# Performance work log

Measured on AMD Instinct MI355X. Metric: run time of the kernel, lower is better.

Reference implementation:

```python
import jax, jax.numpy as jnp
import numpy as np
from jax import ops as jops

N_NODES = 100000
N_EDGES = 1600000
NEG_SLOPE = 0.2
LN_EPS = 1e-5


def setup_inputs() -> dict:
    key = jax.random.key(0)
    ks = jax.random.split(key, 12)
    inp = {
        "x": jax.random.normal(ks[0], (N_NODES, 4), jnp.float32),
        "edge_index": jax.random.randint(ks[1], (2, N_EDGES), 0, N_NODES, jnp.int64 if jax.config.jax_enable_x64 else jnp.int32),
        # layer 1: GATv2Conv(4, 16, heads=4)
        "W1l": jax.random.normal(ks[2], (4, 64), jnp.float32) * 0.5,
        "W1r": jax.random.normal(ks[3], (4, 64), jnp.float32) * 0.5,
        "a1": jax.random.normal(ks[4], (4, 16), jnp.float32) * 0.5,  # [heads, out]
        "b1": jax.random.normal(ks[5], (64,), jnp.float32) * 0.1,
        "g1": jnp.ones((64,), jnp.float32),
        "be1": jnp.zeros((64,), jnp.float32),
        # layer 2: GATv2Conv(64, 32, heads=1)
        "W2l": jax.random.normal(ks[6], (64, 32), jnp.float32) * 0.125,
        "W2r": jax.random.normal(ks[7], (64, 32), jnp.float32) * 0.125,
        "a2": jax.random.normal(ks[8], (1, 32), jnp.float32) * 0.5,
        "b2": jax.random.normal(ks[9], (32,), jnp.float32) * 0.1,
        "g2": jnp.ones((32,), jnp.float32),
        "be2": jnp.zeros((32,), jnp.float32),
    }
    return inp


def _add_self_loops(edge_index, n):
    loop = jnp.arange(n, dtype=edge_index.dtype)
    return jnp.concatenate([edge_index, jnp.stack([loop, loop])], axis=1)


def _gatv2(x, src, dst, Wl, Wr, att, bias, heads, out_ch, n):
    # x: [N, F]; Wl/Wr: [F, heads*out_ch]; att: [heads, out_ch]
    xl = (x @ Wl).reshape(n, heads, out_ch)  # source transform
    xr = (x @ Wr).reshape(n, heads, out_ch)  # target transform
    e = xl[src] + xr[dst]                     # [E, H, C]
    e = jnp.where(e >= 0, e, NEG_SLOPE * e)   # LeakyReLU(0.2)
    logits = jnp.einsum('ehc,hc->eh', e, att)  # [E, H]
    # segment softmax over destination node
    m = jops.segment_max(logits, dst, num_segments=n)  # [N, H]
    ex = jnp.exp(logits - m[dst])
    denom = jops.segment_sum(ex, dst, num_segments=n)  # [N, H]
    alpha = ex / denom[dst]                            # [E, H]
    out = jops.segment_sum(alpha[:, :, None] * xl[src], dst, num_segments=n)  # [N, H, C]
    return out.reshape(n, heads * out_ch) + bias


def _layernorm(x, g, b):
    mu = jnp.mean(x, axis=-1, keepdims=True)
    var = jnp.mean(jnp.square(x - mu), axis=-1, keepdims=True)
    return (x - mu) * jax.lax.rsqrt(var + LN_EPS) * g + b


def reference(x, edge_index, W1l, W1r, a1, b1, g1, be1, W2l, W2r, a2, b2, g2, be2):
    n = x.shape[0]
    ei = _add_self_loops(edge_index, n)
    src, dst = ei[0], ei[1]
    h = _gatv2(x, src, dst, W1l, W1r, a1, b1, heads=4, out_ch=16, n=n)
    h = _layernorm(h, g1, be1)
    h = jnp.where(h > 0, h, jnp.expm1(h))  # ELU
    h = _gatv2(h, src, dst, W2l, W2r, a2, b2, heads=1, out_ch=32, n=n)
    h = _layernorm(h, g2, be2)
    return h
```

## Files before the change

### kernel.cpp

```cpp
#include <hip/hip_runtime.h>
#include <math.h>

#define NN 100000
#define E0 1600000
#define ETOT (E0 + NN)
#define NEG 0.2f

#define NB 512
#define BS 196
#define CHUNK 4096
#define PPT 16
#define MAXP 4096

__device__ __forceinline__ float leaky(float v) { return fmaxf(v, NEG * v); }

__global__ void k_bhist(const int* __restrict__ ei, int* __restrict__ bcnt) {
    __shared__ int h[NB];
    int tid = threadIdx.x;
    for (int i = tid; i < NB; i += 256) h[i] = 0;
    __syncthreads();
    int stride = gridDim.x * 256;
    for (int e = blockIdx.x * 256 + tid; e < E0; e += stride)
        atomicAdd(&h[ei[E0 + e] / BS], 1);
    __syncthreads();
    for (int i = tid; i < NB; i += 256)
        if (h[i]) atomicAdd(&bcnt[i], h[i]);
}

__global__ void k_bscan(const int* __restrict__ bcnt, int* __restrict__ boff,
                        int* __restrict__ srcsBase, int* __restrict__ cursor) {
    __shared__ int s[NB];
    int tid = threadIdx.x;
    int v = bcnt[tid];
    s[tid] = v;
    __syncthreads();
    for (int off = 1; off < NB; off <<= 1) {
        int t = (tid >= off) ? s[tid - off] : 0;
        __syncthreads();
        s[tid] += t;
        __syncthreads();
    }
    int excl = s[tid] - v;
    boff[tid] = excl;
    cursor[tid] = excl;
    int n0 = tid * BS;
    if (n0 > NN) n0 = NN;
    srcsBase[tid] = excl + n0;
}

__global__ void k_bin(const int* __restrict__ ei, int* __restrict__ cursor,
                      int2* __restrict__ binned) {
    __shared__ int hist[NB];
    __shared__ int basesh[NB];
    int tid = threadIdx.x;
    long long cbase = (long long)blockIdx.x * CHUNK;
    for (int i = tid; i < NB; i += 256) hist[i] = 0;
    __syncthreads();
    int srcv[PPT], dstv[PPT], rank[PPT], bkt[PPT];
#pragma unroll
    for (int k = 0; k < PPT; ++k) {
        long long e = cbase + k * 256 + tid;
        if (e < E0) {
            int s_ = ei[e];
            int d_ = ei[E0 + e];
            int b = d_ / BS;
            rank[k] = atomicAdd(&hist[b], 1);
            srcv[k] = s_;
            dstv[k] = d_;
            bkt[k] = b;
        } else {
            bkt[k] = -1;
        }
    }
    __syncthreads();
    for (int i = tid; i < NB; i += 256)
        if (hist[i] > 0) basesh[i] = atomicAdd(&cursor[i], hist[i]);
    __syncthreads();
#pragma unroll
    for (int k = 0; k < PPT; ++k)
        if (bkt[k] >= 0) {
            int2 p;
            p.x = srcv[k];
            p.y = dstv[k];
            binned[basesh[bkt[k]] + rank[k]] = p;
        }
}

__global__ void k_bfin(const int2* __restrict__ binned, const int* __restrict__ bcnt,
                       const int* __restrict__ boff, const int* __restrict__ srcsBase,
                       int* __restrict__ rs, int* __restrict__ srcs) {
    int b = blockIdx.x;
    int n0 = b * BS;
    if (n0 >= NN) return;
    int nd = NN - n0;
    if (nd > BS) nd = BS;
    int cnt = bcnt[b];
    if (cnt > MAXP) cnt = MAXP;
    int base = boff[b];
    int sb = srcsBase[b];
    __shared__ int ldsCnt[256];
    __shared__ int scanA[256];
    __shared__ int rowOffE[256];
    __shared__ int stage[MAXP + BS];
    int tid = threadIdx.x;
    ldsCnt[tid] = 0;
    __syncthreads();
    int srcv[PPT], dl_[PPT], rk_[PPT];
#pragma unroll
    for (int k = 0; k < PPT; ++k) {
        int i = k * 256 + tid;
        if (i < cnt) {
            int2 p = binned[base + i];
            int dl = p.y - n0;
            rk_[k] = atomicAdd(&ldsCnt[dl], 1);
            srcv[k] = p.x;
            dl_[k] = dl;
        } else {
            dl_[k] = -1;
        }
    }
    __syncthreads();
    int v = (tid < nd) ? ldsCnt[tid] + 1 : 0;
    scanA[tid] = v;
    __syncthreads();
    for (int off = 1; off < 256; off <<= 1) {
        int t = (tid >= off) ? scanA[tid - off] : 0;
        __syncthreads();
        scanA[tid] += t;
        __syncthreads();
    }
    rowOffE[tid] = scanA[tid] - v;
    __syncthreads();
    if (tid < nd) {
        int e = rowOffE[tid];
        rs[n0 + tid] = sb + e;
        stage[e] = n0 + tid;
    }
    __syncthreads();
#pragma unroll
    for (int k = 0; k < PPT; ++k)
        if (dl_[k] >= 0) stage[rowOffE[dl_[k]] + 1 + rk_[k]] = srcv[k];
    __syncthreads();
    int tot = cnt + nd;
    for (int i = tid; i < tot; i += 256) srcs[sb + i] = stage[i];
}

__global__ void k_linr(const float* __restrict__ x, const float* __restrict__ Wr,
                       float* __restrict__ xr1) {
    int t = blockIdx.x * blockDim.x + threadIdx.x;
    if (t >= NN * 16) return;
    int n = t >> 4;
    int j = (t & 15) << 2;
    const float4 xv = *(const float4*)(x + (long long)n * 4);
    float4 a = {0.f, 0.f, 0.f, 0.f};
#pragma unroll
    for (int k = 0; k < 4; ++k) {
        float4 w = *(const float4*)(Wr + k * 64 + j);
        float xk = k == 0 ? xv.x : k == 1 ? xv.y : k == 2 ? xv.z : xv.w;
        a.x += xk * w.x; a.y += xk * w.y;
        a.z += xk * w.z; a.w += xk * w.w;
    }
    *(float4*)(xr1 + (long long)n * 64 + j) = a;
}

__global__ void k_gat1(
        const float* __restrict__ x, const float* __restrict__ Wl,
        const float* __restrict__ xr1, const float* __restrict__ att,
        const int* __restrict__ rs, const int* __restrict__ srcs,
        const float* __restrict__ b, const float* __restrict__ g,
        const float* __restrict__ be, float* __restrict__ h) {
    int lane = threadIdx.x & 63;
    int wave = (blockIdx.x * blockDim.x + threadIdx.x) >> 6;
    int nwaves = (gridDim.x * blockDim.x) >> 6;
    int e_i = lane >> 3;
    int sub = lane & 7;
    float wl[4][8], at[8];
#pragma unroll
    for (int k = 0; k < 4; ++k)
#pragma unroll
        for (int j = 0; j < 8; ++j) wl[k][j] = Wl[k * 64 + sub * 8 + j];
#pragma unroll
    for (int j = 0; j < 8; ++j) at[j] = att[sub * 8 + j];

    for (int n = wave; n < NN; n += nwaves) {
        const float4 r0 = *(const float4*)(xr1 + (long long)n * 64 + sub * 8);
        const float4 r1 = *(const float4*)(xr1 + (long long)n * 64 + sub * 8 + 4);
        float xrd[8] = {r0.x, r0.y, r0.z, r0.w, r1.x, r1.y, r1.z, r1.w};
        int beg = rs[n];
        int end = (n == NN - 1) ? ETOT : rs[n + 1];
        float acc4[4] = {0.f, 0.f, 0.f, 0.f};
        float den = 0.f;
        int slot = beg + e_i;
        bool valid = slot < end;
        int s = srcs[valid ? slot : beg];
        float4 xa = *(const float4*)(x + (long long)s * 4);
        for (int base = beg; base < end; base += 8) {
            int nslot = base + 8 + e_i;
            bool nvalid = nslot < end;
            int ns = srcs[nvalid ? nslot : beg];
            float4 xn = *(const float4*)(x + (long long)ns * 4);
            float p = 0.f;
#pragma unroll
            for (int j = 0; j < 8; ++j) {
                float t = xa.x * wl[0][j] + xa.y * wl[1][j] + xa.z * wl[2][j] +
                          xa.w * wl[3][j];
                float u = t + xrd[j];
                u = fmaxf(u, NEG * u);
                p += u * at[j];
            }
            p += __shfl_xor(p, 1);
            float ex = valid ? __expf(p) : 0.f;
            den += ex;
            acc4[0] += ex * xa.x;
            acc4[1] += ex * xa.y;
            acc4[2] += ex * xa.z;
            acc4[3] += ex * xa.w;
            xa = xn;
            valid = nvalid;
        }
#pragma unroll
        for (int m = 8; m <= 32; m <<= 1) {
#pragma unroll
            for (int k = 0; k < 4; ++k) acc4[k] += __shfl_xor(acc4[k], m);
            den += __shfl_xor(den, m);
        }
        int cf = sub * 8 + e_i;
        float v = (acc4[0] * Wl[cf] + acc4[1] * Wl[64 + cf] +
                   acc4[2] * Wl[128 + cf] + acc4[3] * Wl[192 + cf]) / den + b[cf];
        float s1 = v;
#pragma unroll
        for (int m = 1; m < 64; m <<= 1) s1 += __shfl_xor(s1, m);
        float mu = s1 * (1.f / 64.f);
        float c = v - mu;
        float sq = c * c;
#pragma unroll
        for (int m = 1; m < 64; m <<= 1) sq += __shfl_xor(sq, m);
        float y = c * rsqrtf(sq * (1.f / 64.f) + 1e-5f) * g[cf] + be[cf];
        h[(long long)n * 64 + cf] = y > 0.f ? y : expm1f(y);
    }
}

__global__ void k_lin2(const float* __restrict__ h, const float* __restrict__ Wl,
                       const float* __restrict__ Wr, float* __restrict__ xl2,
                       float* __restrict__ xr2) {
    __shared__ float wl_s[2048];
    __shared__ float wr_s[2048];
    for (int i = threadIdx.x; i < 2048; i += blockDim.x) {
        wl_s[i] = Wl[i];
        wr_s[i] = Wr[i];
    }
    __syncthreads();
    int t = blockIdx.x * blockDim.x + threadIdx.x;
    if (t >= NN * 32) return;
    int n = t >> 5, j = t & 31;
    const float* hr = h + (long long)n * 64;
    float al = 0.f, ar = 0.f;
#pragma unroll 8
    for (int k = 0; k < 64; ++k) {
        float hv = hr[k];
        al += hv * wl_s[k * 32 + j];
        ar += hv * wr_s[k * 32 + j];
    }
    xl2[(long long)n * 32 + j] = al;
    xr2[(long long)n * 32 + j] = ar;
}

__global__ void k_gat2(
        const float* __restrict__ xl2, const float* __restrict__ xr2,
        const float* __restrict__ att, const int* __restrict__ rs,
        const int* __restrict__ srcs, const float* __restrict__ b,
        const float* __restrict__ g, const float* __restrict__ be,
        float* __restrict__ out) {
    int lane = threadIdx.x & 63;
    int wave = (blockIdx.x * blockDim.x + threadIdx.x) >> 6;
    int nwaves = (gridDim.x * blockDim.x) >> 6;
    int e_i = lane >> 3;
    int cg = lane & 7;
    float at[4];
#pragma unroll
    for (int j = 0; j < 4; ++j) at[j] = att[cg * 4 + j];

    for (int n = wave; n < NN; n += nwaves) {
        const float4 xr4 = *(const float4*)(xr2 + (long long)n * 32 + cg * 4);
        float xrd[4] = {xr4.x, xr4.y, xr4.z, xr4.w};
        int beg = rs[n];
        int end = (n == NN - 1) ? ETOT : rs[n + 1];
        float acc[4] = {0.f, 0.f, 0.f, 0.f};
        float den = 0.f;
        int slot = beg + e_i;
        bool valid = slot < end;
        int s = srcs[valid ? slot : beg];
        float4 xa = *(const float4*)(xl2 + (long long)s * 32 + cg * 4);
        for (int base = beg; base < end; base += 8) {
            int nslot = base + 8 + e_i;
            bool nvalid = nslot < end;
            int ns = srcs[nvalid ? nslot : beg];
            float4 xn = *(const float4*)(xl2 + (long long)ns * 32 + cg * 4);
            float p = 0.f;
#pragma unroll
            for (int j = 0; j < 4; ++j) {
                float xls = j == 0 ? xa.x : j == 1 ? xa.y : j == 2 ? xa.z : xa.w;
                float u = xls + xrd[j];
                u = fmaxf(u, NEG * u);
                p += u * at[j];
            }
            p += __shfl_xor(p, 1);
            p += __shfl_xor(p, 2);
            p += __shfl_xor(p, 4);
            float ex = valid ? __expf(p) : 0.f;
            den += ex;
            acc[0] += ex * xa.x;
            acc[1] += ex * xa.y;
            acc[2] += ex * xa.z;
            acc[3] += ex * xa.w;
            xa = xn;
            valid = nvalid;
        }
#pragma unroll
        for (int m = 8; m <= 32; m <<= 1) {
#pragma unroll
            for (int j = 0; j < 4; ++j) acc[j] += __shfl_xor(acc[j], m);
            den += __shfl_xor(den, m);
        }
        int e3 = e_i & 3;
        float v = acc[0];
#pragma unroll
        for (int j = 1; j < 4; ++j) v = (e3 == j) ? acc[j] : v;
        int cf = cg * 4 + e3;
        v = v / den + b[cf];
        float s1 = v;
#pragma unroll
        for (int m = 1; m < 64; m <<= 1) s1 += __shfl_xor(s1, m);
        float mu = s1 * (1.f / 64.f);
        float cc = v - mu;
        float sq = cc * cc;
#pragma unroll
        for (int m = 1; m < 64; m <<= 1) sq += __shfl_xor(sq, m);
        float y = cc * rsqrtf(sq * (1.f / 64.f) + 1e-5f) * g[cf] + be[cf];
        if (e_i < 4) out[(long long)n * 32 + cf] = y;
    }
}

extern "C" void kernel_launch(void* const* d_in, const int* in_sizes, int n_in,
                              void* d_out, int out_size, void* d_ws, size_t ws_size,
                              hipStream_t stream) {
    const float* x   = (const float*)d_in[0];
    const int*   ei  = (const int*)d_in[1];
    const float* W1l = (const float*)d_in[2];
    const float* W1r = (const float*)d_in[3];
    const float* a1  = (const float*)d_in[4];
    const float* b1  = (const float*)d_in[5];
    const float* g1  = (const float*)d_in[6];
    const float* be1 = (const float*)d_in[7];
    const float* W2l = (const float*)d_in[8];
    const float* W2r = (const float*)d_in[9];
    const float* a2  = (const float*)d_in[10];
    const float* b2  = (const float*)d_in[11];
    const float* g2  = (const float*)d_in[12];
    const float* be2 = (const float*)d_in[13];
    float* out = (float*)d_out;

    float* ws = (float*)d_ws;
    float* h   = ws;
    float* xr1 = ws + 6400000;
    float* xl2 = ws + 6400000;
    float* xr2 = ws + 9600000;
    int2* binned = (int2*)ws;
    int* ib        = (int*)(ws + 12800000);
    int* rs        = ib;
    int* srcs      = ib + 100000;
    int* bcnt      = ib + 1800000;
    int* boff      = ib + 1800000 + NB;
    int* srcsBase  = ib + 1800000 + 2 * NB;
    int* cursor    = ib + 1800000 + 3 * NB;

    hipMemsetAsync(bcnt, 0, NB * sizeof(int), stream);
    k_bhist<<<256, 256, 0, stream>>>(ei, bcnt);
    k_bscan<<<1, NB, 0, stream>>>(bcnt, boff, srcsBase, cursor);
    k_bin<<<(E0 + CHUNK - 1) / CHUNK, 256, 0, stream>>>(ei, cursor, binned);
    k_bfin<<<NB, 256, 0, stream>>>(binned, bcnt, boff, srcsBase, rs, srcs);
    k_linr<<<(NN * 16 + 255) / 256, 256, 0, stream>>>(x, W1r, xr1);

    k_gat1<<<2048, 256, 0, stream>>>(x, W1l, xr1, a1, rs, srcs, b1, g1, be1, h);
    k_lin2<<<(NN * 32 + 255) / 256, 256, 0, stream>>>(h, W2l, W2r, xl2, xr2);
    k_gat2<<<2048, 256, 0, stream>>>(xl2, xr2, a2, rs, srcs, b2, g2, be2, out);
}
```

Before: 239.1 us.

## Use packed FP32 math and prescaled source offsets in GAT edge loops

Rewrites the per-edge inner loops of both GAT kernels to use v_pk_fma/v_pk_mul/v_pk_add on float pairs, roughly halving the VALU instruction count for the projection, LeakyReLU and accumulation. Source indices are stored prescaled by 16 so gather addresses need no multiply. A sentinel rs[NN] is added to remove the last-node branch, and srcs is padded with zeroed entries so the prefetch can read past the end without clamping. This trades inline asm and workspace offset changes for fewer ALU and address ops in the gather-bound loops.

```diff
diff --git a/kernel.cpp b/kernel.cpp
--- a/kernel.cpp
+++ b/kernel.cpp
@@ -12,7 +12,29 @@
 #define PPT 16
 #define MAXP 4096
 
-__device__ __forceinline__ float leaky(float v) { return fmaxf(v, NEG * v); }
+typedef __attribute__((ext_vector_type(2))) float f32x2;
+
+__device__ __forceinline__ f32x2 pk_fma(f32x2 a, f32x2 b, f32x2 c) {
+    f32x2 d;
+    asm("v_pk_fma_f32 %0, %1, %2, %3" : "=v"(d) : "v"(a), "v"(b), "v"(c));
+    return d;
+}
+__device__ __forceinline__ f32x2 pk_mul(f32x2 a, f32x2 b) {
+    f32x2 d;
+    asm("v_pk_mul_f32 %0, %1, %2" : "=v"(d) : "v"(a), "v"(b));
+    return d;
+}
+__device__ __forceinline__ f32x2 pk_add(f32x2 a, f32x2 b) {
+    f32x2 d;
+    asm("v_pk_add_f32 %0, %1, %2" : "=v"(d) : "v"(a), "v"(b));
+    return d;
+}
+__device__ __forceinline__ f32x2 pk_max(f32x2 a, f32x2 b) {
+    f32x2 d;
+    d[0] = fmaxf(a[0], b[0]);
+    d[1] = fmaxf(a[1], b[1]);
+    return d;
+}
 
 __global__ void k_bhist(const int* __restrict__ ei, int* __restrict__ bcnt) {
     __shared__ int h[NB];
@@ -28,7 +50,8 @@
 }
 
 __global__ void k_bscan(const int* __restrict__ bcnt, int* __restrict__ boff,
-                        int* __restrict__ srcsBase, int* __restrict__ cursor) {
+                        int* __restrict__ srcsBase, int* __restrict__ cursor,
+                        int* __restrict__ rs) {
     __shared__ int s[NB];
     int tid = threadIdx.x;
     int v = bcnt[tid];
@@ -46,6 +69,7 @@
     int n0 = tid * BS;
     if (n0 > NN) n0 = NN;
     srcsBase[tid] = excl + n0;
+    if (tid == 0) rs[NN] = ETOT;
 }
 
 __global__ void k_bin(const int* __restrict__ ei, int* __restrict__ cursor,
@@ -142,7 +166,7 @@
         if (dl_[k] >= 0) stage[rowOffE[dl_[k]] + 1 + rk_[k]] = srcv[k];
     __syncthreads();
     int tot = cnt + nd;
-    for (int i = tid; i < tot; i += 256) srcs[sb + i] = stage[i];
+    for (int i = tid; i < tot; i += 256) srcs[sb + i] = stage[i] << 4;
 }
 
 __global__ void k_linr(const float* __restrict__ x, const float* __restrict__ Wr,
@@ -166,7 +190,7 @@
 __global__ void k_gat1(
         const float* __restrict__ x, const float* __restrict__ Wl,
         const float* __restrict__ xr1, const float* __restrict__ att,
-        const int* __restrict__ rs, const int* __restrict__ srcs,
+        const int* __restrict__ rs, const int* __restrict__ srcs16,
         const float* __restrict__ b, const float* __restrict__ g,
         const float* __restrict__ be, float* __restrict__ h) {
     int lane = threadIdx.x & 63;
@@ -174,50 +198,61 @@
     int nwaves = (gridDim.x * blockDim.x) >> 6;
     int e_i = lane >> 3;
     int sub = lane & 7;
-    float wl[4][8], at[8];
+    f32x2 wl2[4][4], at2[4];
 #pragma unroll
     for (int k = 0; k < 4; ++k)
 #pragma unroll
-        for (int j = 0; j < 8; ++j) wl[k][j] = Wl[k * 64 + sub * 8 + j];
-#pragma unroll
-    for (int j = 0; j < 8; ++j) at[j] = att[sub * 8 + j];
+        for (int jp = 0; jp < 4; ++jp)
+            wl2[k][jp] = *(const f32x2*)(Wl + k * 64 + sub * 8 + jp * 2);
+#pragma unroll
+    for (int jp = 0; jp < 4; ++jp)
+        at2[jp] = *(const f32x2*)(att + sub * 8 + jp * 2);
+    const f32x2 neg2 = {NEG, NEG};
+    const char* xb = (const char*)x;
 
     for (int n = wave; n < NN; n += nwaves) {
-        const float4 r0 = *(const float4*)(xr1 + (long long)n * 64 + sub * 8);
-        const float4 r1 = *(const float4*)(xr1 + (long long)n * 64 + sub * 8 + 4);
-        float xrd[8] = {r0.x, r0.y, r0.z, r0.w, r1.x, r1.y, r1.z, r1.w};
+        f32x2 xrd2[4];
+#pragma unroll
+        for (int jp = 0; jp < 4; ++jp)
+            xrd2[jp] = *(const f32x2*)(xr1 + (long long)n * 64 + sub * 8 + jp * 2);
         int beg = rs[n];
-        int end = (n == NN - 1) ? ETOT : rs[n + 1];
-        float acc4[4] = {0.f, 0.f, 0.f, 0.f};
+        int end = rs[n + 1];
+        int rem = end - beg;
+        const int* sp = srcs16 + beg + e_i;
+        int left = rem - e_i;
+        f32x2 acc01 = {0.f, 0.f}, acc23 = {0.f, 0.f};
         float den = 0.f;
-        int slot = beg + e_i;
-        bool valid = slot < end;
-        int s = srcs[valid ? slot : beg];
-        float4 xa = *(const float4*)(x + (long long)s * 4);
-        for (int base = beg; base < end; base += 8) {
-            int nslot = base + 8 + e_i;
-            bool nvalid = nslot < end;
-            int ns = srcs[nvalid ? nslot : beg];
-            float4 xn = *(const float4*)(x + (long long)ns * 4);
-            float p = 0.f;
-#pragma unroll
-            for (int j = 0; j < 8; ++j) {
-                float t = xa.x * wl[0][j] + xa.y * wl[1][j] + xa.z * wl[2][j] +
-                          xa.w * wl[3][j];
-                float u = t + xrd[j];
-                u = fmaxf(u, NEG * u);
-                p += u * at[j];
+        int s16 = sp[0];
+        float4 xa = *(const float4*)(xb + (unsigned)s16);
+        int nit = (rem + 7) >> 3;
+        for (int it = 0; it < nit; ++it) {
+            int s16n = sp[8];
+            sp += 8;
+            float4 xn = *(const float4*)(xb + (unsigned)s16n);
+            f32x2 xx = {xa.x, xa.x}, xy = {xa.y, xa.y};
+            f32x2 xz = {xa.z, xa.z}, xw = {xa.w, xa.w};
+            f32x2 p2 = {0.f, 0.f};
+#pragma unroll
+            for (int jp = 0; jp < 4; ++jp) {
+                f32x2 t = pk_fma(xx, wl2[0][jp], xrd2[jp]);
+                t = pk_fma(xy, wl2[1][jp], t);
+                t = pk_fma(xz, wl2[2][jp], t);
+                t = pk_fma(xw, wl2[3][jp], t);
+                f32x2 u = pk_max(t, pk_mul(t, neg2));
+                p2 = pk_fma(u, at2[jp], p2);
             }
+            float p = p2[0] + p2[1];
             p += __shfl_xor(p, 1);
-            float ex = valid ? __expf(p) : 0.f;
+            float ex = (left > 0) ? __expf(p) : 0.f;
+            left -= 8;
             den += ex;
-            acc4[0] += ex * xa.x;
-            acc4[1] += ex * xa.y;
-            acc4[2] += ex * xa.z;
-            acc4[3] += ex * xa.w;
+            f32x2 ee = {ex, ex};
+            f32x2 a01 = {xa.x, xa.y}, a23 = {xa.z, xa.w};
+            acc01 = pk_fma(ee, a01, acc01);
+            acc23 = pk_fma(ee, a23, acc23);
             xa = xn;
-            valid = nvalid;
-        }
+        }
+        float acc4[4] = {acc01[0], acc01[1], acc23[0], acc23[1]};
 #pragma unroll
         for (int m = 8; m <= 32; m <<= 1) {
 #pragma unroll
@@ -268,7 +303,7 @@
 __global__ void k_gat2(
         const float* __restrict__ xl2, const float* __restrict__ xr2,
         const float* __restrict__ att, const int* __restrict__ rs,
-        const int* __restrict__ srcs, const float* __restrict__ b,
+        const int* __restrict__ srcs16, const float* __restrict__ b,
         const float* __restrict__ g, const float* __restrict__ be,
         float* __restrict__ out) {
     int lane = threadIdx.x & 63;
@@ -276,46 +311,49 @@
     int nwaves = (gridDim.x * blockDim.x) >> 6;
     int e_i = lane >> 3;
     int cg = lane & 7;
-    float at[4];
-#pragma unroll
-    for (int j = 0; j < 4; ++j) at[j] = att[cg * 4 + j];
+    f32x2 at2[2];
+    at2[0] = *(const f32x2*)(att + cg * 4);
+    at2[1] = *(const f32x2*)(att + cg * 4 + 2);
+    const f32x2 neg2 = {NEG, NEG};
+    const char* xlb = (const char*)xl2 + cg * 16;
 
     for (int n = wave; n < NN; n += nwaves) {
-        const float4 xr4 = *(const float4*)(xr2 + (long long)n * 32 + cg * 4);
-        float xrd[4] = {xr4.x, xr4.y, xr4.z, xr4.w};
+        f32x2 xrd0 = *(const f32x2*)(xr2 + (long long)n * 32 + cg * 4);
+        f32x2 xrd1 = *(const f32x2*)(xr2 + (long long)n * 32 + cg * 4 + 2);
         int beg = rs[n];
-        int end = (n == NN - 1) ? ETOT : rs[n + 1];
-        float acc[4] = {0.f, 0.f, 0.f, 0.f};
+        int end = rs[n + 1];
+        int rem = end - beg;
+        const int* sp = srcs16 + beg + e_i;
+        int left = rem - e_i;
+        f32x2 acc01 = {0.f, 0.f}, acc23 = {0.f, 0.f};
         float den = 0.f;
-        int slot = beg + e_i;
-        bool valid = slot < end;
-        int s = srcs[valid ? slot : beg];
-        float4 xa = *(const float4*)(xl2 + (long long)s * 32 + cg * 4);
-        for (int base = beg; base < end; base += 8) {
-            int nslot = base + 8 + e_i;
-            bool nvalid = nslot < end;
-            int ns = srcs[nvalid ? nslot : beg];
-            float4 xn = *(const float4*)(xl2 + (long long)ns * 32 + cg * 4);
-            float p = 0.f;
-#pragma unroll
-            for (int j = 0; j < 4; ++j) {
-                float xls = j == 0 ? xa.x : j == 1 ? xa.y : j == 2 ? xa.z : xa.w;
-                float u = xls + xrd[j];
-                u = fmaxf(u, NEG * u);
-                p += u * at[j];
-            }
+        int s16 = sp[0];
+        float4 xa = *(const float4*)(xlb + (unsigned)(s16 << 3));
+        int nit = (rem + 7) >> 3;
+        for (int it = 0; it < nit; ++it) {
+            int s16n = sp[8];
+            sp += 8;
+            float4 xn = *(const float4*)(xlb + (unsigned)(s16n << 3));
+            f32x2 a01 = {xa.x, xa.y}, a23 = {xa.z, xa.w};
+            f32x2 t0 = pk_add(a01, xrd0);
+            f32x2 t1 = pk_add(a23, xrd1);
+            f32x2 u0 = pk_max(t0, pk_mul(t0, neg2));
+            f32x2 u1 = pk_max(t1, pk_mul(t1, neg2));
+            f32x2 p2 = pk_mul(u0, at2[0]);
+            p2 = pk_fma(u1, at2[1], p2);
+            float p = p2[0] + p2[1];
             p += __shfl_xor(p, 1);
             p += __shfl_xor(p, 2);
             p += __shfl_xor(p, 4);
-            float ex = valid ? __expf(p) : 0.f;
+            float ex = (left > 0) ? __expf(p) : 0.f;
+            left -= 8;
             den += ex;
-            acc[0] += ex * xa.x;
-            acc[1] += ex * xa.y;
-            acc[2] += ex * xa.z;
-            acc[3] += ex * xa.w;
+            f32x2 ee = {ex, ex};
+            acc01 = pk_fma(ee, a01, acc01);
+            acc23 = pk_fma(ee, a23, acc23);
             xa = xn;
-            valid = nvalid;
-        }
+        }
+        float acc[4] = {acc01[0], acc01[1], acc23[0], acc23[1]};
 #pragma unroll
         for (int m = 8; m <= 32; m <<= 1) {
 #pragma unroll
@@ -368,15 +406,16 @@
     int2* binned = (int2*)ws;
     int* ib        = (int*)(ws + 12800000);
     int* rs        = ib;
-    int* srcs      = ib + 100000;
-    int* bcnt      = ib + 1800000;
-    int* boff      = ib + 1800000 + NB;
-    int* srcsBase  = ib + 1800000 + 2 * NB;
-    int* cursor    = ib + 1800000 + 3 * NB;
+    int* srcs      = ib + 100001;
+    int* bcnt      = ib + 1800100;
+    int* boff      = ib + 1800100 + NB;
+    int* srcsBase  = ib + 1800100 + 2 * NB;
+    int* cursor    = ib + 1800100 + 3 * NB;
 
     hipMemsetAsync(bcnt, 0, NB * sizeof(int), stream);
+    hipMemsetAsync(srcs + ETOT, 0, 64 * sizeof(int), stream);
     k_bhist<<<256, 256, 0, stream>>>(ei, bcnt);
-    k_bscan<<<1, NB, 0, stream>>>(bcnt, boff, srcsBase, cursor);
+    k_bscan<<<1, NB, 0, stream>>>(bcnt, boff, srcsBase, cursor, rs);
     k_bin<<<(E0 + CHUNK - 1) / CHUNK, 256, 0, stream>>>(ei, cursor, binned);
     k_bfin<<<NB, 256, 0, stream>>>(binned, bcnt, boff, srcsBase, rs, srcs);
     k_linr<<<(NN * 16 + 255) / 256, 256, 0, stream>>>(x, W1r, xr1);
```

Measured after the change: 258.1 us. 8.0% more time.
